# Optimization experiments

Hardware: AMD Instinct MI355X
Metric: run time of the kernel (lower is better)

The kernel has to match this reference:

```python
import jax, jax.numpy as jnp
import numpy as np

D_MODEL = 1024
NUM_HEADS = 16
ROPE_THETA = 10000.0


def _rope(v, pos, theta=ROPE_THETA):
    # v: [B, S, D] (full d_model, as in the original module), pos: [B, S] int
    d = v.shape[-1]
    inv_freq = theta ** (-jnp.arange(0, d, 2, dtype=jnp.float32) / d)  # [D/2]
    ang = pos.astype(jnp.float32)[..., None] * inv_freq  # [B, S, D/2]
    cos, sin = jnp.cos(ang), jnp.sin(ang)
    x1, x2 = v[..., ::2], v[..., 1::2]
    r1 = x1 * cos - x2 * sin
    r2 = x1 * sin + x2 * cos
    return jnp.stack([r1, r2], axis=-1).reshape(v.shape)


def setup_inputs() -> dict:
    key = jax.random.key(0)
    ks = jax.random.split(key, 6)
    B, S, D = 2, 2048, D_MODEL
    std = np.sqrt(2.0 / (D + D)).astype(np.float32)
    x = jax.random.normal(ks[0], (B, S, D), dtype=jnp.float32)
    token_positions = jnp.sort(jax.random.randint(ks[1], (B, S), 0, S), axis=-1).astype(jnp.int32)
    wq = jax.random.normal(ks[2], (D, D), dtype=jnp.float32) * std
    wk = jax.random.normal(ks[3], (D, D), dtype=jnp.float32) * std
    wv = jax.random.normal(ks[4], (D, D), dtype=jnp.float32) * std
    wo = jax.random.normal(ks[5], (D, D), dtype=jnp.float32) * std
    return {"x": x, "token_positions": token_positions, "wq": wq, "wk": wk, "wv": wv, "wo": wo}


def reference(x, token_positions, wq, wk, wv, wo):
    B, S, D = x.shape
    H = NUM_HEADS
    dk = D // H
    # Projections (nn.functional.linear: x @ W^T)
    q = x @ wq.T
    k = x @ wk.T
    v = x @ wv.T
    # In the original, Q/K are reshaped to heads and back before RoPE -> identity;
    # RoPE is applied over the FULL d_model dimension.
    q = _rope(q, token_positions)
    k = _rope(k, token_positions)
    # Split heads
    q = q.reshape(B, S, H, dk)
    k = k.reshape(B, S, H, dk)
    v = v.reshape(B, S, H, dk)
    scores = jnp.einsum('bqhd,bkhd->bhqk', q, k) / jnp.sqrt(jnp.asarray(dk, x.dtype))
    causal = jnp.tril(jnp.ones((S, S), dtype=bool))  # True where allowed
    scores = jnp.where(causal[None, None], scores, -jnp.inf)
    attn = jax.nn.softmax(scores, axis=-1)
    out = jnp.einsum('bhqk,bkhd->bqhd', attn, v).reshape(B, S, D)
    return out @ wo.T
```

## Files before the change

### kernel.cpp

```cpp
#include <hip/hip_runtime.h>
#include <hip/hip_bf16.h>
#include <math.h>

typedef __attribute__((ext_vector_type(8))) short bf16x8;
typedef __attribute__((ext_vector_type(4))) short short4x;
typedef __attribute__((ext_vector_type(4))) float f32x4;
typedef __attribute__((ext_vector_type(8))) float f32x8;

#define D_MODEL 1024
#define NHEADS  16
#define DK      64
#define BATCH   2
#define SEQ     2048

static __device__ __forceinline__ short f2bf(float f) {
    unsigned u = __builtin_bit_cast(unsigned, f);
    u = u + 0x7FFFu + ((u >> 16) & 1u);
    return (short)(u >> 16);
}
static __device__ __forceinline__ short f2bf_fast(float f) {
    return (short)((__builtin_bit_cast(unsigned, f) + 0x8000u) >> 16);
}
static __device__ __forceinline__ float bf2f(short s) {
    return __builtin_bit_cast(float, ((unsigned)(unsigned short)s) << 16);
}

typedef __attribute__((address_space(3))) unsigned int lds_uint;
typedef __attribute__((address_space(1))) const unsigned int glob_uint;
static __device__ __forceinline__ void gl2lds16(const short* g, short* l) {
    __builtin_amdgcn_global_load_lds((glob_uint*)g, (lds_uint*)l, 16, 0, 0);
}

#define NX8 ((BATCH * SEQ * D_MODEL) / 8)
#define NW8 ((D_MODEL * D_MODEL) / 8)
__global__ void cvt_all_kernel(const void* __restrict__ x,  const void* __restrict__ wq,
                               const void* __restrict__ wk, const void* __restrict__ wv,
                               const void* __restrict__ wo,
                               __hip_bfloat16* __restrict__ xb,  __hip_bfloat16* __restrict__ wqb,
                               __hip_bfloat16* __restrict__ wkb, __hip_bfloat16* __restrict__ wvb,
                               __hip_bfloat16* __restrict__ wob,
                               int* __restrict__ dtf)
{
    __shared__ int sflag;
    if (threadIdx.x < 64) {
        const unsigned w = ((const unsigned*)x)[threadIdx.x];
        const unsigned e = (w >> 7) & 0xFFu;
        const bool weird = (e >= 0x88u) || (e <= 0x5Fu);
        const unsigned long long m = __ballot(weird);
        if (threadIdx.x == 0) {
            const int f = (__popcll(m) >= 16) ? 1 : 0;
            sflag = f;
            if (blockIdx.x == 0) *dtf = f;
        }
    }
    __syncthreads();

    const int i = blockIdx.x * blockDim.x + threadIdx.x;
    if (i >= NX8 + 4 * NW8) return;
    const void* src; __hip_bfloat16* dst; int off;
    if (i < NX8) { src = x; dst = xb; off = i; }
    else {
        const int j = i - NX8, seg = j >> 17; off = j & (NW8 - 1);
        switch (seg) {
            case 0: src = wq; dst = wqb; break;
            case 1: src = wk; dst = wkb; break;
            case 2: src = wv; dst = wvb; break;
            default: src = wo; dst = wob; break;
        }
    }
    if (sflag) {
        const f32x8 v = ((const f32x8*)src)[off];
        bf16x8 r;
#pragma unroll
        for (int j = 0; j < 8; ++j) r[j] = f2bf(v[j]);
        ((bf16x8*)dst)[off] = r;
    } else {
        ((bf16x8*)dst)[off] = ((const bf16x8*)src)[off];
    }
}

static __device__ __forceinline__ void gemm128_main(
    const short* __restrict__ A, const short* __restrict__ B,
    int K, int bm, int bn, f32x4 (&acc)[4][4], short* lds)
{
    const int tid  = threadIdx.x;
    const int lane = tid & 63;
    const int wave = tid >> 6;
    const int l16  = lane & 15;
    const int quad = lane >> 4;

    const int srow = lane >> 2;
    const int scg  = (lane & 3) ^ ((lane >> 3) & 3);
    const short* ag = A + (size_t)(bm + wave * 32 + srow) * K + scg * 8;
    const short* bg = B + (size_t)(bn + wave * 32 + srow) * K + scg * 8;
    const int dst = wave * 1024 + lane * 8;

    const int mrow = (wave >> 1) * 64;
    const int nrow = (wave & 1) * 64;
    const int ph   = ((quad ^ ((l16 >> 1) & 3))) * 8;

    auto stage = [&](int k0, int buf) {
        short* ad = lds + buf * 4096 + dst;
        short* bd = lds + 8192 + buf * 4096 + dst;
        gl2lds16(ag + k0, ad);
        gl2lds16(ag + k0 + (size_t)16 * K, ad + 512);
        gl2lds16(bg + k0, bd);
        gl2lds16(bg + k0 + (size_t)16 * K, bd + 512);
    };

    stage(0, 0);
    for (int k0 = 0, t = 0; k0 < K; k0 += 32, ++t) {
        __asm__ volatile("s_waitcnt vmcnt(0)" ::: "memory");
        __syncthreads();
        if (k0 + 32 < K) stage(k0 + 32, (t + 1) & 1);

        const short* Ab = lds + (t & 1) * 4096;
        const short* Bb = lds + 8192 + (t & 1) * 4096;
        bf16x8 a[4], b[4];
#pragma unroll
        for (int x = 0; x < 4; ++x)
            a[x] = *(const bf16x8*)(Ab + (mrow + x * 16 + l16) * 32 + ph);
#pragma unroll
        for (int y = 0; y < 4; ++y)
            b[y] = *(const bf16x8*)(Bb + (nrow + y * 16 + l16) * 32 + ph);
#pragma unroll
        for (int x = 0; x < 4; ++x)
#pragma unroll
            for (int y = 0; y < 4; ++y)
                acc[x][y] = __builtin_amdgcn_mfma_f32_16x16x32_bf16(
                    a[x], b[y], acc[x][y], 0, 0, 0);
    }
}

__global__ __launch_bounds__(256) void gemm_qkv_kernel(
    const __hip_bfloat16* __restrict__ xb,
    const __hip_bfloat16* __restrict__ wqb,
    const __hip_bfloat16* __restrict__ wkb,
    const __hip_bfloat16* __restrict__ wvb,
    const int* __restrict__ pos,
    __hip_bfloat16* __restrict__ Qb,
    __hip_bfloat16* __restrict__ Kb,
    __hip_bfloat16* __restrict__ Vt)
{
    __shared__ alignas(16) short lds[16384];
    const int wsel = blockIdx.x >> 3;
    const int bn   = (blockIdx.x & 7) * 128;
    const int bm   = blockIdx.y * 128;
    const short* W = (const short*)(wsel == 0 ? wqb : (wsel == 1 ? wkb : wvb));

    f32x4 acc[4][4];
#pragma unroll
    for (int x = 0; x < 4; ++x)
#pragma unroll
        for (int y = 0; y < 4; ++y) acc[x][y] = (f32x4){0.f, 0.f, 0.f, 0.f};

    gemm128_main((const short*)xb, W, D_MODEL, bm, bn, acc, lds);

    const int lane = threadIdx.x & 63;
    const int wave = threadIdx.x >> 6;
    const int l16  = lane & 15;
    const int quad = lane >> 4;

    if (wsel == 2) {
#pragma unroll
        for (int x = 0; x < 4; ++x)
#pragma unroll
            for (int y = 0; y < 4; ++y)
#pragma unroll
                for (int r = 0; r < 4; ++r) {
                    const int row = bm + (wave >> 1) * 64 + x * 16 + quad * 4 + r;
                    const int col = bn + (wave & 1) * 64 + y * 16 + l16;
                    const int hh = col >> 6, dcol = col & 63;
                    const int bb = row >> 11, ss = row & (SEQ - 1);
                    Vt[(((size_t)bb * NHEADS + hh) * DK + dcol) * SEQ + ss] =
                        __float2bfloat16(acc[x][y][r]);
                }
        return;
    }

    __hip_bfloat16* Crm = (wsel == 1) ? Kb : Qb;
    const float qscale = (wsel == 0) ? 0.18033688011f : 1.0f;
#pragma unroll
    for (int x = 0; x < 4; ++x)
#pragma unroll
        for (int r = 0; r < 4; ++r) {
            const int row = bm + (wave >> 1) * 64 + x * 16 + quad * 4 + r;
            const float p = (float)pos[row];
#pragma unroll
            for (int y = 0; y < 4; ++y) {
                const int col = bn + (wave & 1) * 64 + y * 16 + l16;
                const float inv = exp2f((float)(col >> 1) * -0.02595256257f);
                const float ang = p * inv;
                const float c = __cosf(ang), s = __sinf(ang);
                const float v  = acc[x][y][r];
                const float pv = __shfl_xor(v, 1);
                const float vr = v * c + pv * ((l16 & 1) ? s : -s);
                Crm[(size_t)row * D_MODEL + col] = __float2bfloat16(vr * qscale);
            }
        }
}

__global__ __launch_bounds__(256) void gemm_out_kernel(
    const __hip_bfloat16* __restrict__ AO,
    const __hip_bfloat16* __restrict__ wob,
    void* __restrict__ C, const int* __restrict__ dtf)
{
    __shared__ alignas(16) short lds[2][6144];
    const int tid  = threadIdx.x;
    const int lane = tid & 63;
    const int wave = tid >> 6;
    const int l16  = lane & 15;
    const int quad = lane >> 4;
    const int bn = blockIdx.x * 128;
    const int bm = blockIdx.y * 64;
    const bool c32 = (*dtf) != 0;
    const int K = D_MODEL;

    const int srow = lane >> 2;
    const int scg  = (lane & 3) ^ ((lane >> 3) & 3);
    const short* Ap = (const short*)AO;
    const short* Bp = (const short*)wob;
    const short* ag = Ap + (size_t)(bm + wave * 16 + srow) * K + scg * 8;
    const short* bg = Bp + (size_t)(bn + wave * 32 + srow) * K + scg * 8;

    const int nrow = wave * 32;
    const int ph   = ((quad ^ ((l16 >> 1) & 3))) * 8;

    f32x4 acc[4][2];
#pragma unroll
    for (int x = 0; x < 4; ++x)
#pragma unroll
        for (int y = 0; y < 2; ++y) acc[x][y] = (f32x4){0.f, 0.f, 0.f, 0.f};

    auto stage = [&](int k0, int buf) {
        gl2lds16(ag + k0, &lds[buf][wave * 512 + lane * 8]);
        gl2lds16(bg + k0, &lds[buf][2048 + wave * 1024 + lane * 8]);
        gl2lds16(bg + k0 + (size_t)16 * K, &lds[buf][2048 + wave * 1024 + 512 + lane * 8]);
    };

    stage(0, 0);
    for (int k0 = 0, t = 0; k0 < K; k0 += 32, ++t) {
        __asm__ volatile("s_waitcnt vmcnt(0)" ::: "memory");
        __syncthreads();
        if (k0 + 32 < K) stage(k0 + 32, (t + 1) & 1);

        const short* Ab = &lds[t & 1][0];
        const short* Bb = &lds[t & 1][2048];
        bf16x8 a[4], b[2];
#pragma unroll
        for (int x = 0; x < 4; ++x)
            a[x] = *(const bf16x8*)(Ab + (x * 16 + l16) * 32 + ph);
#pragma unroll
        for (int y = 0; y < 2; ++y)
            b[y] = *(const bf16x8*)(Bb + (nrow + y * 16 + l16) * 32 + ph);
#pragma unroll
        for (int x = 0; x < 4; ++x)
#pragma unroll
            for (int y = 0; y < 2; ++y)
                acc[x][y] = __builtin_amdgcn_mfma_f32_16x16x32_bf16(
                    a[x], b[y], acc[x][y], 0, 0, 0);
    }

#pragma unroll
    for (int x = 0; x < 4; ++x)
#pragma unroll
        for (int y = 0; y < 2; ++y)
#pragma unroll
            for (int r = 0; r < 4; ++r) {
                const int row = bm + x * 16 + quad * 4 + r;
                const int col = bn + nrow + y * 16 + l16;
                const size_t idx = (size_t)row * D_MODEL + col;
                if (c32) ((float*)C)[idx] = acc[x][y][r];
                else     ((__hip_bfloat16*)C)[idx] = __float2bfloat16(acc[x][y][r]);
            }
}

__global__ __launch_bounds__(256, 2) void flash_attn_kernel(
    __hip_bfloat16* QO,
    const __hip_bfloat16* __restrict__ Kt,
    const __hip_bfloat16* __restrict__ Vt)
{
    __shared__ alignas(16) char pool[66560];
    short* k_lds = (short*)pool;
    short* v_lds = (short*)(pool + 32768);

    const int lane = threadIdx.x & 63;
    const int wave = threadIdx.x >> 6;
    const int l16  = lane & 15;
    const int quad = lane >> 4;
    const int qt   = 31 - blockIdx.y;
    const int bh   = blockIdx.x;
    const int b    = bh >> 4;
    const int h    = bh & 15;
    const size_t base  = (size_t)b * SEQ * D_MODEL + h * DK;
    const size_t vbase = (size_t)bh * DK * SEQ;

    const short* Qp = (const short*)QO;
    const short* Kp = (const short*)Kt;
    const short* Vp = (const short*)Vt;

    bf16x8 aq[4][2];
#pragma unroll
    for (int qf = 0; qf < 4; ++qf)
#pragma unroll
        for (int ks = 0; ks < 2; ++ks)
            aq[qf][ks] = *(const bf16x8*)(Qp + base +
                (size_t)(qt * 64 + qf * 16 + l16) * D_MODEL + ks * 32 + quad * 8);

    f32x4 o[4][4];
    float ls[4] = {0.f, 0.f, 0.f, 0.f};
#pragma unroll
    for (int qf = 0; qf < 4; ++qf)
#pragma unroll
        for (int nf = 0; nf < 4; ++nf) o[qf][nf] = (f32x4){0.f, 0.f, 0.f, 0.f};

    const int srow = lane >> 3;
    const int scg  = (lane & 7) ^ srow;
    const short* kg = Kp + ((size_t)b * SEQ + wave * 32 + srow) * D_MODEL + h * DK + scg * 8;
    const int ge = (l16 & 8) | ((l16 & 7) ^ quad);
    const int go = (l16 & 8) | ((l16 & 7) ^ (4 + quad));
    const short* vgA = Vp + vbase + (size_t)(wave * 16 + quad) * SEQ + ge * 8;
    const short* vgB = Vp + vbase + (size_t)(wave * 16 + 4 + quad) * SEQ + go * 8;

    auto stage = [&](int t, int buf) {
        const int kv0 = t * 128;
        short* kd = k_lds + buf * 8192 + (wave * 32) * 64 + lane * 8;
#pragma unroll
        for (int i = 0; i < 4; ++i)
            gl2lds16(kg + (size_t)(kv0 + i * 8) * D_MODEL, kd + i * 8 * 64);
        short* vd = v_lds + buf * 8192 + (wave * 16) * 128 + lane * 8;
        gl2lds16(vgA + kv0,                 vd);
        gl2lds16(vgB + kv0,                 vd + 4 * 128);
        gl2lds16(vgA + (size_t)8 * SEQ + kv0, vd + 8 * 128);
        gl2lds16(vgB + (size_t)8 * SEQ + kv0, vd + 12 * 128);
    };

    auto compute = [&](int buf, int kv0, bool tail) {
        const short* kb = k_lds + buf * 8192;
        const short* vb = v_lds + buf * 8192;
        bf16x8 ak[2][2];
#pragma unroll
        for (int kvf = 0; kvf < 2; ++kvf)
#pragma unroll
            for (int ks = 0; ks < 2; ++ks) {
                const int row = wave * 32 + kvf * 16 + l16;
                const int g = (ks * 4 + quad) ^ (l16 & 7);
                ak[kvf][ks] = *(const bf16x8*)(kb + row * 64 + g * 8);
            }
        f32x4 s[2][4];
        __builtin_amdgcn_s_setprio(1);
#pragma unroll
        for (int kvf = 0; kvf < 2; ++kvf)
#pragma unroll
            for (int qf = 0; qf < 4; ++qf) {
                f32x4 c = (f32x4){0.f, 0.f, 0.f, 0.f};
                c = __builtin_amdgcn_mfma_f32_16x16x32_bf16(ak[kvf][0], aq[qf][0], c, 0, 0, 0);
                c = __builtin_amdgcn_mfma_f32_16x16x32_bf16(ak[kvf][1], aq[qf][1], c, 0, 0, 0);
                s[kvf][qf] = c;
            }
        __builtin_amdgcn_s_setprio(0);

        bf16x8 pa[4];
#pragma unroll
        for (int qf = 0; qf < 4; ++qf) {
            const int qrow = qt * 64 + qf * 16 + l16;
#pragma unroll
            for (int kvf = 0; kvf < 2; ++kvf)
#pragma unroll
                for (int r = 0; r < 4; ++r) {
                    float p = exp2f(s[kvf][qf][r]);
                    if (tail && (kv0 + wave * 32 + kvf * 16 + quad * 4 + r > qrow))
                        p = 0.f;
                    ls[qf] += p;
                    pa[qf][kvf * 4 + r] = f2bf_fast(p);
                }
        }

        if (tail) { __asm__ volatile("s_waitcnt vmcnt(0)" ::: "memory"); }
        else      { __asm__ volatile("s_waitcnt vmcnt(8)" ::: "memory"); }
        __builtin_amdgcn_s_barrier();

        bf16x8 bv[4];
#pragma unroll
        for (int nf = 0; nf < 4; ++nf) {
            const int d = nf * 16 + l16;
#pragma unroll
            for (int e = 0; e < 2; ++e) {
                const int g  = wave * 4 + e * 2 + (quad >> 1);
                const int gs = (g & 8) | ((g & 7) ^ (l16 & 7));
                const short4x v4 = *(const short4x*)(vb + d * 128 + gs * 8 + (quad & 1) * 4);
                bv[nf][e * 4 + 0] = v4[0];
                bv[nf][e * 4 + 1] = v4[1];
                bv[nf][e * 4 + 2] = v4[2];
                bv[nf][e * 4 + 3] = v4[3];
            }
        }
        __builtin_amdgcn_s_setprio(1);
#pragma unroll
        for (int qf = 0; qf < 4; ++qf)
#pragma unroll
            for (int nf = 0; nf < 4; ++nf)
                o[qf][nf] = __builtin_amdgcn_mfma_f32_16x16x32_bf16(
                    pa[qf], bv[nf], o[qf][nf], 0, 0, 0);
        __builtin_amdgcn_s_setprio(0);
    };

    const int tmax = qt >> 1;
    stage(0, 0);
    for (int t = 0; t < tmax; ++t) {
        __asm__ volatile("s_waitcnt vmcnt(4)" ::: "memory");
        __syncthreads();
        stage(t + 1, (t + 1) & 1);
        compute(t & 1, t * 128, false);
    }
    __asm__ volatile("s_waitcnt vmcnt(4)" ::: "memory");
    __syncthreads();
    compute(tmax & 1, tmax * 128, true);

#pragma unroll
    for (int qf = 0; qf < 4; ++qf) {
        ls[qf] += __shfl_xor(ls[qf], 16);
        ls[qf] += __shfl_xor(ls[qf], 32);
    }
    __syncthreads();
    float* red = (float*)pool;
    float* lsb = (float*)(pool + 65536);
#pragma unroll
    for (int qf = 0; qf < 4; ++qf)
#pragma unroll
        for (int nf = 0; nf < 4; ++nf)
            *(f32x4*)(red + ((wave * 16 + qf * 4 + nf) * 64 + lane) * 4) = o[qf][nf];
    if (quad == 0)
#pragma unroll
        for (int qf = 0; qf < 4; ++qf) lsb[wave * 64 + qf * 16 + l16] = ls[qf];
    __syncthreads();

    f32x4 lden = (f32x4){0.f, 0.f, 0.f, 0.f};
#pragma unroll
    for (int w = 0; w < 4; ++w)
        lden += *(const f32x4*)(lsb + w * 64 + wave * 16 + quad * 4);
    f32x4 osum[4];
#pragma unroll
    for (int nf = 0; nf < 4; ++nf) {
        f32x4 a = (f32x4){0.f, 0.f, 0.f, 0.f};
#pragma unroll
        for (int w = 0; w < 4; ++w)
            a += *(const f32x4*)(red + ((w * 16 + wave * 4 + nf) * 64 + lane) * 4);
        osum[nf] = a;
    }
    float inv[4];
#pragma unroll
    for (int r = 0; r < 4; ++r) inv[r] = 1.f / fmaxf(lden[r], 1e-20f);
#pragma unroll
    for (int nf = 0; nf < 4; ++nf)
#pragma unroll
        for (int r = 0; r < 4; ++r)
            QO[base + (size_t)(qt * 64 + wave * 16 + quad * 4 + r) * D_MODEL
                    + nf * 16 + l16]
                = __float2bfloat16(osum[nf][r] * inv[r]);
}

extern "C" void kernel_launch(void* const* d_in, const int* in_sizes, int n_in,
                              void* d_out, int out_size, void* d_ws, size_t ws_size,
                              hipStream_t stream)
{
    (void)in_sizes; (void)n_in; (void)out_size; (void)ws_size;

    const void* x  = d_in[0];
    const int*  pos = (const int*)d_in[1];
    const void* wq = d_in[2];
    const void* wk = d_in[3];
    const void* wv = d_in[4];
    const void* wo = d_in[5];

    const int M = BATCH * SEQ;
    const int D = D_MODEL;
    const size_t MD = (size_t)M * D;
    const size_t DD = (size_t)D * D;

    int* dtf = (int*)d_ws;
    __hip_bfloat16* xb  = (__hip_bfloat16*)((char*)d_ws + 256);
    __hip_bfloat16* wqb = xb  + MD;
    __hip_bfloat16* wkb = wqb + DD;
    __hip_bfloat16* wvb = wkb + DD;
    __hip_bfloat16* wob = wvb + DD;
    __hip_bfloat16* Qb  = wob + DD;
    __hip_bfloat16* Vtb = Qb  + MD;
    __hip_bfloat16* Kb  = (__hip_bfloat16*)d_out;

    dim3 blk(256);

    const int ncvt = NX8 + 4 * NW8;
    hipLaunchKernelGGL(cvt_all_kernel, dim3((ncvt + 255) / 256), blk, 0, stream,
                       x, wq, wk, wv, wo, xb, wqb, wkb, wvb, wob, dtf);

    hipLaunchKernelGGL(gemm_qkv_kernel, dim3(24, 32), blk, 0, stream,
                       xb, wqb, wkb, wvb, pos, Qb, Kb, Vtb);

    hipLaunchKernelGGL(flash_attn_kernel, dim3(32, 32), blk, 0, stream,
                       Qb, Kb, Vtb);

    hipLaunchKernelGGL(gemm_out_kernel, dim3(D / 128, M / 64), blk, 0, stream,
                       Qb, wob, d_out, dtf);
}
```

Measured before the change: 178.9 us.

## Fuse Q and K projections into one block sharing the staged X tile

Q and K projection blocks now compute both outputs from the same X tile in shared memory. Each block stages X, Wq and Wk tiles with double buffering and runs two sets of MFMA accumulators. V blocks stay separate, so the grid shrinks from 24 to 16 columns. This halves X tile loads for Q/K but doubles accumulator registers and grows LDS to 48KB, which may reduce occupancy and leave the Q/K blocks unbalanced against the V blocks.

```diff
diff --git a/kernel.cpp b/kernel.cpp
--- a/kernel.cpp
+++ b/kernel.cpp
@@ -142,26 +142,23 @@
     __hip_bfloat16* __restrict__ Kb,
     __hip_bfloat16* __restrict__ Vt)
 {
-    __shared__ alignas(16) short lds[16384];
-    const int wsel = blockIdx.x >> 3;
-    const int bn   = (blockIdx.x & 7) * 128;
-    const int bm   = blockIdx.y * 128;
-    const short* W = (const short*)(wsel == 0 ? wqb : (wsel == 1 ? wkb : wvb));
-
-    f32x4 acc[4][4];
-#pragma unroll
-    for (int x = 0; x < 4; ++x)
-#pragma unroll
-        for (int y = 0; y < 4; ++y) acc[x][y] = (f32x4){0.f, 0.f, 0.f, 0.f};
-
-    gemm128_main((const short*)xb, W, D_MODEL, bm, bn, acc, lds);
-
-    const int lane = threadIdx.x & 63;
-    const int wave = threadIdx.x >> 6;
+    __shared__ alignas(16) short lds[24576];
+    const int tid  = threadIdx.x;
+    const int lane = tid & 63;
+    const int wave = tid >> 6;
     const int l16  = lane & 15;
     const int quad = lane >> 4;
-
-    if (wsel == 2) {
+    const int bm   = blockIdx.y * 128;
+    const int K    = D_MODEL;
+
+    if (blockIdx.x >= 8) {
+        const int bn = (blockIdx.x - 8) * 128;
+        f32x4 acc[4][4];
+#pragma unroll
+        for (int x = 0; x < 4; ++x)
+#pragma unroll
+            for (int y = 0; y < 4; ++y) acc[x][y] = (f32x4){0.f, 0.f, 0.f, 0.f};
+        gemm128_main((const short*)xb, (const short*)wvb, K, bm, bn, acc, lds);
 #pragma unroll
         for (int x = 0; x < 4; ++x)
 #pragma unroll
@@ -178,26 +175,94 @@
         return;
     }
 
-    __hip_bfloat16* Crm = (wsel == 1) ? Kb : Qb;
-    const float qscale = (wsel == 0) ? 0.18033688011f : 1.0f;
+    const int bn = blockIdx.x * 128;
+    const int srow = lane >> 2;
+    const int scg  = (lane & 3) ^ ((lane >> 3) & 3);
+    const short* ag = (const short*)xb  + (size_t)(bm + wave * 32 + srow) * K + scg * 8;
+    const short* qg = (const short*)wqb + (size_t)(bn + wave * 32 + srow) * K + scg * 8;
+    const short* kg = (const short*)wkb + (size_t)(bn + wave * 32 + srow) * K + scg * 8;
+    const int dst = wave * 1024 + lane * 8;
+
+    const int mrow = (wave >> 1) * 64;
+    const int nrow = (wave & 1) * 64;
+    const int ph   = ((quad ^ ((l16 >> 1) & 3))) * 8;
+
+    f32x4 accq[4][4], acck[4][4];
 #pragma unroll
     for (int x = 0; x < 4; ++x)
 #pragma unroll
-        for (int r = 0; r < 4; ++r) {
-            const int row = bm + (wave >> 1) * 64 + x * 16 + quad * 4 + r;
-            const float p = (float)pos[row];
-#pragma unroll
-            for (int y = 0; y < 4; ++y) {
-                const int col = bn + (wave & 1) * 64 + y * 16 + l16;
-                const float inv = exp2f((float)(col >> 1) * -0.02595256257f);
-                const float ang = p * inv;
-                const float c = __cosf(ang), s = __sinf(ang);
-                const float v  = acc[x][y][r];
-                const float pv = __shfl_xor(v, 1);
-                const float vr = v * c + pv * ((l16 & 1) ? s : -s);
-                Crm[(size_t)row * D_MODEL + col] = __float2bfloat16(vr * qscale);
+        for (int y = 0; y < 4; ++y) {
+            accq[x][y] = (f32x4){0.f, 0.f, 0.f, 0.f};
+            acck[x][y] = (f32x4){0.f, 0.f, 0.f, 0.f};
+        }
+
+    auto stage = [&](int k0, int buf) {
+        short* ad = lds +         buf * 4096 + dst;
+        short* qd = lds +  8192 + buf * 4096 + dst;
+        short* kd = lds + 16384 + buf * 4096 + dst;
+        gl2lds16(ag + k0, ad);
+        gl2lds16(ag + k0 + (size_t)16 * K, ad + 512);
+        gl2lds16(qg + k0, qd);
+        gl2lds16(qg + k0 + (size_t)16 * K, qd + 512);
+        gl2lds16(kg + k0, kd);
+        gl2lds16(kg + k0 + (size_t)16 * K, kd + 512);
+    };
+
+    stage(0, 0);
+    for (int k0 = 0, t = 0; k0 < K; k0 += 32, ++t) {
+        __asm__ volatile("s_waitcnt vmcnt(0)" ::: "memory");
+        __syncthreads();
+        if (k0 + 32 < K) stage(k0 + 32, (t + 1) & 1);
+
+        const short* Ab  = lds +         (t & 1) * 4096;
+        const short* Bqb = lds +  8192 + (t & 1) * 4096;
+        const short* Bkb = lds + 16384 + (t & 1) * 4096;
+        bf16x8 a[4], b[4];
+#pragma unroll
+        for (int x = 0; x < 4; ++x)
+            a[x] = *(const bf16x8*)(Ab + (mrow + x * 16 + l16) * 32 + ph);
+#pragma unroll
+        for (int y = 0; y < 4; ++y)
+            b[y] = *(const bf16x8*)(Bqb + (nrow + y * 16 + l16) * 32 + ph);
+#pragma unroll
+        for (int x = 0; x < 4; ++x)
+#pragma unroll
+            for (int y = 0; y < 4; ++y)
+                accq[x][y] = __builtin_amdgcn_mfma_f32_16x16x32_bf16(
+                    a[x], b[y], accq[x][y], 0, 0, 0);
+#pragma unroll
+        for (int y = 0; y < 4; ++y)
+            b[y] = *(const bf16x8*)(Bkb + (nrow + y * 16 + l16) * 32 + ph);
+#pragma unroll
+        for (int x = 0; x < 4; ++x)
+#pragma unroll
+            for (int y = 0; y < 4; ++y)
+                acck[x][y] = __builtin_amdgcn_mfma_f32_16x16x32_bf16(
+                    a[x], b[y], acck[x][y], 0, 0, 0);
+    }
+
+    auto rope_write = [&](f32x4 (&acc)[4][4], __hip_bfloat16* Crm, float qscale) {
+#pragma unroll
+        for (int x = 0; x < 4; ++x)
+#pragma unroll
+            for (int r = 0; r < 4; ++r) {
+                const int row = bm + (wave >> 1) * 64 + x * 16 + quad * 4 + r;
+                const float p = (float)pos[row];
+#pragma unroll
+                for (int y = 0; y < 4; ++y) {
+                    const int col = bn + (wave & 1) * 64 + y * 16 + l16;
+                    const float inv = exp2f((float)(col >> 1) * -0.02595256257f);
+                    const float ang = p * inv;
+                    const float c = __cosf(ang), s = __sinf(ang);
+                    const float v  = acc[x][y][r];
+                    const float pv = __shfl_xor(v, 1);
+                    const float vr = v * c + pv * ((l16 & 1) ? s : -s);
+                    Crm[(size_t)row * D_MODEL + col] = __float2bfloat16(vr * qscale);
+                }
             }
-        }
+    };
+    rope_write(accq, Qb, 0.18033688011f);
+    rope_write(acck, Kb, 1.0f);
 }
 
 __global__ __launch_bounds__(256) void gemm_out_kernel(
@@ -494,7 +559,7 @@
     hipLaunchKernelGGL(cvt_all_kernel, dim3((ncvt + 255) / 256), blk, 0, stream,
                        x, wq, wk, wv, wo, xb, wqb, wkb, wvb, wob, dtf);
 
-    hipLaunchKernelGGL(gemm_qkv_kernel, dim3(24, 32), blk, 0, stream,
+    hipLaunchKernelGGL(gemm_qkv_kernel, dim3(16, 32), blk, 0, stream,
                        xb, wqb, wkb, wvb, pos, Qb, Kb, Vtb);
 
     hipLaunchKernelGGL(flash_attn_kernel, dim3(32, 32), blk, 0, stream,
```

Result: slower. 185.6 us (+3.7%).
